# Kernel tuning notes

Measured on AMD Instinct MI355X. Metric: run time of the kernel, lower is better.

## Reference

```python
import jax, jax.numpy as jnp
import numpy as np

# ---- fixed config (Linear_mvm defaults, XBAR 64x64) ----
ROW = 64; COL = 64
BIT_SLICE = 2; BIT_STREAM = 1
W_BITS = 16; W_FRAC = 12          # weight_bit_frac = weight_bits//4*3
I_BITS = 16; I_FRAC = 12          # input_bit_frac  = input_bits//4*3
ADC_BIT = 8                       # log2(ROW) + bit_slice (bit_stream==1)
ACM_BITS = 16; ACM_FRAC = 12
BSN = W_BITS // BIT_SLICE         # 8 slices per weight, MSB-first columns
STN = I_BITS // BIT_STREAM        # 16 input bit-streams, LSB-first
IN_F = 1024; OUT_F = 1024; BATCH = 256


def _bit_slice_weight(w_nonneg):
    # w_nonneg: [out, in] nonnegative -> sliced crossbar matrix [in, out*BSN] (MSB->LSB per channel)
    w_int = jnp.clip(jnp.round(w_nonneg * (2.0 ** W_FRAC)), 0.0, 2.0 ** W_BITS - 1.0)
    shifts = (BIT_SLICE * (BSN - 1 - jnp.arange(BSN))).astype(jnp.float32)
    sl = jnp.floor(w_int[..., None] / (2.0 ** shifts)) % (2 ** BIT_SLICE)  # [out,in,BSN]
    o, i = w_nonneg.shape
    return sl.transpose(1, 0, 2).reshape(i, o * BSN)


def _input_bits(x):
    # two's-complement fixed point, LSB-first bit planes: [b, in, STN]
    x_int = jnp.clip(jnp.round(x * (2.0 ** I_FRAC)), -(2.0 ** (I_BITS - 1)), 2.0 ** (I_BITS - 1) - 1.0)
    x_u = jnp.where(x_int < 0, x_int + 2.0 ** I_BITS, x_int)
    return jnp.floor(x_u[..., None] / (2.0 ** jnp.arange(I_BITS, dtype=jnp.float32))) % 2.0


def _tile(mat, r, c):
    # pad to tile multiples and reshape to [xr, xc, r, c]
    pr = (-mat.shape[0]) % r; pc = (-mat.shape[1]) % c
    m = jnp.pad(mat, ((0, pr), (0, pc)))
    xr, xc = m.shape[0] // r, m.shape[1] // c
    return m.reshape(xr, r, xc, c).transpose(0, 2, 1, 3)


def _adc(a):
    # uniform ADC quantization of the analog column current to ADC_BIT bits
    full = float(ROW * (2 ** BIT_SLICE - 1))
    step = full / (2.0 ** ADC_BIT - 1.0)
    return jnp.clip(jnp.round(a / step) * step, 0.0, full)


def _mvm_one_sign(bits_tiled, xbars):
    # bits_tiled [b, xr, ROW, STN]; xbars [xr, xc, ROW, COL]
    sw_slice = 2.0 ** (BIT_SLICE * (BSN - 1 - jnp.arange(BSN, dtype=jnp.float32)))  # MSB..LSB
    sw_stream = 2.0 ** (BIT_STREAM * jnp.arange(STN, dtype=jnp.float32))
    sw_stream = sw_stream.at[-1].multiply(-1.0)  # two's-complement MSB stream

    def step(acc, si):
        bi, w = si                                   # bi [b,xr,ROW]
        analog = jnp.einsum('brk,rckj->brcj', bi, xbars)  # [b,xr,xc,COL]
        analog = _adc(analog)
        b, xr, xc, _ = analog.shape
        dig = analog.reshape(b, xr, xc, COL // BSN, BSN) @ sw_slice  # shift-add slices
        return acc + w * dig, None

    b = bits_tiled.shape[0]; xr, xc = xbars.shape[0], xbars.shape[1]
    acc0 = jnp.zeros((b, xr, xc, COL // BSN), jnp.float32)
    streams = jnp.moveaxis(bits_tiled, -1, 0)  # [STN, b, xr, ROW]
    acc, _ = jax.lax.scan(step, acc0, (streams, sw_stream))
    return acc.sum(axis=1).reshape(b, xc * (COL // BSN))  # sum row tiles, flatten channels


def _forward(x, weight, bias):
    pos = _bit_slice_weight(jnp.maximum(weight, 0.0))
    neg = _bit_slice_weight(-jnp.minimum(weight, 0.0))
    xb_pos = _tile(pos, ROW, COL)
    xb_neg = _tile(neg, ROW, COL)
    bits = _input_bits(x)                                  # [b,in,STN]
    xr = xb_pos.shape[0]
    bits = jnp.pad(bits, ((0, 0), (0, xr * ROW - bits.shape[1]), (0, 0)))
    bits = bits.reshape(x.shape[0], xr, ROW, STN)
    out = _mvm_one_sign(bits, xb_pos) - _mvm_one_sign(bits, xb_neg)
    out = out * (2.0 ** (-(W_FRAC + I_FRAC)))              # undo fixed-point scaling
    # accumulator quantization to ACM_BITS / ACM_FRAC
    out = jnp.clip(jnp.round(out * 2.0 ** ACM_FRAC), -(2.0 ** (ACM_BITS - 1)), 2.0 ** (ACM_BITS - 1) - 1.0) * 2.0 ** (-ACM_FRAC)
    out = out[:, :OUT_F]
    return out + bias[None, :]


def setup_inputs() -> dict:
    key = jax.random.key(0)
    k1, k2, k3 = jax.random.split(key, 3)
    x = jax.random.normal(k1, (BATCH, IN_F), jnp.float32)
    weight = jax.random.normal(k2, (OUT_F, IN_F), jnp.float32) * 0.05  # representable in Q4.12
    bias = jax.random.normal(k3, (OUT_F,), jnp.float32) * 0.05
    return {"x": x, "weight": weight, "bias": bias}


def reference(x, weight, bias):
    return _forward(x, weight, bias)
```

## Files before the change

### kernel.cpp

```cpp
#include <hip/hip_runtime.h>
#include <stdint.h>

#define BATCH 256
#define IN_F  1024
#define OUT_F 1024
#define RT    16
#define STN   16
#define NCOL  16384

typedef int   v4i  __attribute__((ext_vector_type(4)));
typedef int   v16i __attribute__((ext_vector_type(16)));
typedef float v2f  __attribute__((ext_vector_type(2)));

#define AP_SZ ((size_t)STN * BATCH * IN_F)
#define BP_SZ ((size_t)64 * NCOL * 16)

__global__ __launch_bounds__(256) void pack_fused(
    const float* __restrict__ x, const float* __restrict__ w,
    uint8_t* __restrict__ Ap2, uint8_t* __restrict__ Bp,
    uint32_t* __restrict__ flags)
{
    if (blockIdx.x < 512) {
        int item = blockIdx.x * 256 + threadIdx.x;
        int o  = item & 1023;
        int sg = (item >> 10) & 1;
        int g  = item >> 11;
        const float* wr = w + (size_t)o * IN_F + g * 16;
        uint32_t wq[16];
        #pragma unroll
        for (int j = 0; j < 16; ++j) {
            float wv = wr[j];
            float wf = rintf(fmaxf(sg ? -wv : wv, 0.0f) * 4096.0f);
            wq[j] = (uint32_t)fminf(wf, 65535.0f);
        }
        uint32_t nzmask = 0;
        #pragma unroll
        for (int s = 0; s < 8; ++s) {
            int sh = 14 - 2 * s;
            uint32_t dw[4], nz = 0;
            #pragma unroll
            for (int q = 0; q < 4; ++q) {
                uint32_t d = 0;
                #pragma unroll
                for (int j = 0; j < 4; ++j)
                    d |= ((wq[q * 4 + j] >> sh) & 3u) << (8 * j);
                dw[q] = d;
                nz |= d;
            }
            int sgs = sg * 8 + s;
            *(uint4*)(Bp + (size_t)(g * NCOL + sgs * 1024 + o) * 16) =
                make_uint4(dw[0], dw[1], dw[2], dw[3]);
            nzmask |= (nz ? 1u : 0u) << s;
        }
        int r = g >> 2, ob = o >> 7;
        #pragma unroll
        for (int s = 0; s < 8; ++s) {
            int any = __any((int)((nzmask >> s) & 1u));
            if (any && (threadIdx.x & 63) == 0)
                atomicOr(&flags[(sg * 8 + s) * 8 + ob], 1u << r);
        }
    } else {
        int item = (blockIdx.x - 512) * 256 + threadIdx.x;
        int b  = item & 255;
        int tq = (item >> 8) & 3;
        int kg = item >> 10;
        int r = kg >> 2, f = (kg >> 1) & 1, hi = kg & 1;
        int y = b >> 5, l = hi * 32 + (b & 31);
        const float* xr = x + (size_t)b * IN_F + kg * 16;
        uint32_t xu[16];
        #pragma unroll
        for (int j = 0; j < 16; ++j) {
            float xf = rintf(xr[j] * 4096.0f);
            xf = fminf(fmaxf(xf, -32768.0f), 32767.0f);
            xu[j] = (uint32_t)((int)xf) & 0xFFFFu;
        }
        uint8_t* wbase = Ap2 + ((size_t)(r * 8 + y) * 16) * 2048 + f * 1024 + l * 16;
        #pragma unroll
        for (int tt = 0; tt < 4; ++tt) {
            int t = tq * 4 + tt;
            uint32_t dw[4];
            #pragma unroll
            for (int q = 0; q < 4; ++q) {
                uint32_t d = 0;
                #pragma unroll
                for (int j = 0; j < 4; ++j)
                    d |= ((xu[q * 4 + j] >> t) & 1u) << (8 * j);
                dw[q] = d;
            }
            *(uint4*)(wbase + t * 2048) = make_uint4(dw[0], dw[1], dw[2], dw[3]);
        }
    }
}

__global__ __launch_bounds__(512) void cim_block(
    const uint8_t* __restrict__ Ap2, const uint8_t* __restrict__ Bp,
    const uint32_t* __restrict__ flags, const float* __restrict__ bias,
    float* __restrict__ out)
{
    __shared__ float red[8 * 1024];
    const float MAG = 12582912.0f;
    int tid = threadIdx.x, wid = tid >> 6, l = tid & 63, h2 = l >> 5;
    int oq = blockIdx.x, y = blockIdx.y;
    int ob = oq >> 2;

    uint32_t fw = flags[(l & 15) * 8 + ob];

    v2f acc2[8];
    #pragma unroll
    for (int i = 0; i < 8; ++i) acc2[i] = (v2f)0.0f;
    v16i zero;
    #pragma unroll
    for (int i = 0; i < 16; ++i) zero[i] = 0;

    int cnt = 0;
    for (int r = 0; r < RT; ++r) {
        uint32_t smask = (uint32_t)(__ballot((int)((fw >> r) & 1u))) & 0xFFFFu;
        while (smask) {
            int sgs = __builtin_ctz(smask);
            smask &= smask - 1;
            if ((cnt++ & 7) != wid) continue;

            int s = sgs & 7, sg = sgs >> 3;
            float clane = __int_as_float((141 - 2 * s) << 23) * (192.0f / 255.0f);
            if (sg) clane = -clane;
            int col = sgs * 1024 + oq * 32 + (l & 31);

            v4i bf0 = *(const v4i*)(Bp + ((size_t)(r * 4 + h2)     * NCOL + col) * 16);
            v4i bf1 = *(const v4i*)(Bp + ((size_t)(r * 4 + 2 + h2) * NCOL + col) * 16);

            const uint8_t* abase = Ap2 + ((size_t)(r * 8 + y) * 16) * 2048 + l * 16;
            #pragma unroll 4
            for (int t = 0; t < STN; ++t) {
                const uint8_t* ap = abase + t * 2048;
                v4i af0 = *(const v4i*)ap;
                v4i af1 = *(const v4i*)(ap + 1024);
                v16i c = __builtin_amdgcn_mfma_i32_32x32x32_i8(af0, bf0, zero, 0, 0, 0);
                c      = __builtin_amdgcn_mfma_i32_32x32x32_i8(af1, bf1, c,    0, 0, 0);
                float wt = (t == 15) ? -32768.0f : (float)(1 << t);
                float cw = clane * wt;
                #pragma unroll
                for (int i = 0; i < 8; ++i) {
                    v2f af; af.x = (float)c[2 * i]; af.y = (float)c[2 * i + 1];
                    v2f tq;
                    tq.x = fmaf(af.x, 1.328125f, MAG);
                    tq.y = fmaf(af.y, 1.328125f, MAG);
                    v2f qf = tq - MAG;
                    acc2[i].x = fmaf(qf.x, cw, acc2[i].x);
                    acc2[i].y = fmaf(qf.y, cw, acc2[i].y);
                }
            }
        }
    }

    float* slot = red + wid * 1024 + l * 16;
    #pragma unroll
    for (int i = 0; i < 8; ++i) {
        slot[2 * i]     = acc2[i].x;
        slot[2 * i + 1] = acc2[i].y;
    }
    __syncthreads();
    #pragma unroll
    for (int k = 0; k < 2; ++k) {
        int e = k * 512 + tid;
        float v = 0.0f;
        #pragma unroll
        for (int w = 0; w < 8; ++w) v += red[w * 1024 + e];
        int ll = e >> 4, i = e & 15;
        int b = y * 32 + (i & 3) + 8 * (i >> 2) + 4 * (ll >> 5);
        int o = oq * 32 + (ll & 31);
        float ov = v * 0x1p-24f;
        float q = rintf(ov * 4096.0f);
        q = fminf(fmaxf(q, -32768.0f), 32767.0f);
        out[(size_t)b * OUT_F + o] = q * 0x1p-12f + bias[o];
    }
}

extern "C" void kernel_launch(void* const* d_in, const int* in_sizes, int n_in,
                              void* d_out, int out_size, void* d_ws, size_t ws_size,
                              hipStream_t stream) {
    const float* x    = (const float*)d_in[0];
    const float* w    = (const float*)d_in[1];
    const float* bias = (const float*)d_in[2];
    float* out = (float*)d_out;

    uint8_t*  Ap2   = (uint8_t*)d_ws;
    uint8_t*  Bp    = Ap2 + AP_SZ;
    uint32_t* flags = (uint32_t*)(Bp + BP_SZ);

    hipMemsetAsync(flags, 0, 128 * sizeof(uint32_t), stream);
    hipLaunchKernelGGL(pack_fused, dim3(768), dim3(256), 0, stream,
                       x, w, Ap2, Bp, flags);
    hipLaunchKernelGGL(cim_block, dim3(32, 8), dim3(512), 0, stream,
                       Ap2, Bp, flags, bias, out);
}
```

Measured before the change: 175.3 us.

## Double-buffer input bit planes in LDS and refine sparsity flags to 32-column granularity

The MFMA kernel now stages each row tile's input bit-plane block into double-buffered LDS with global_load_lds, prefetching the next active row tile while computing the current one, instead of reloading A fragments from global memory in every wave. Skip flags move from 128-column to 32-column granularity, so each block tests only its own columns and skips whole row tiles with no nonzero slices. The reduction buffer reuses the LDS staging space with a transposed layout. This adds a block-wide barrier per row tile, which could serialise waves whose work is unbalanced.

```diff
diff --git a/kernel.cpp b/kernel.cpp
--- a/kernel.cpp
+++ b/kernel.cpp
@@ -25,6 +25,7 @@
         int o  = item & 1023;
         int sg = (item >> 10) & 1;
         int g  = item >> 11;
+        int l  = threadIdx.x & 63;
         const float* wr = w + (size_t)o * IN_F + g * 16;
         uint32_t wq[16];
         #pragma unroll
@@ -52,12 +53,14 @@
                 make_uint4(dw[0], dw[1], dw[2], dw[3]);
             nzmask |= (nz ? 1u : 0u) << s;
         }
-        int r = g >> 2, ob = o >> 7;
+        int r = g >> 2;
         #pragma unroll
         for (int s = 0; s < 8; ++s) {
-            int any = __any((int)((nzmask >> s) & 1u));
-            if (any && (threadIdx.x & 63) == 0)
-                atomicOr(&flags[(sg * 8 + s) * 8 + ob], 1u << r);
+            unsigned long long bal = __ballot((int)((nzmask >> s) & 1u));
+            uint32_t lo = (uint32_t)bal, hi = (uint32_t)(bal >> 32);
+            int sgs = sg * 8 + s;
+            if (l == 0 && lo)  atomicOr(&flags[sgs * 32 + (o >> 5)], 1u << r);
+            if (l == 32 && hi) atomicOr(&flags[sgs * 32 + (o >> 5)], 1u << r);
         }
     } else {
         int item = (blockIdx.x - 512) * 256 + threadIdx.x;
@@ -97,13 +100,16 @@
     const uint32_t* __restrict__ flags, const float* __restrict__ bias,
     float* __restrict__ out)
 {
-    __shared__ float red[8 * 1024];
+    __shared__ __align__(16) uint8_t Abuf[2][32768];
     const float MAG = 12582912.0f;
     int tid = threadIdx.x, wid = tid >> 6, l = tid & 63, h2 = l >> 5;
     int oq = blockIdx.x, y = blockIdx.y;
-    int ob = oq >> 2;
-
-    uint32_t fw = flags[(l & 15) * 8 + ob];
+
+    uint32_t fw = flags[(l & 15) * 32 + oq];
+    uint32_t rmask = fw;
+    #pragma unroll
+    for (int st = 1; st < 16; st <<= 1)
+        rmask |= __shfl_xor(rmask, st, 64);
 
     v2f acc2[8];
     #pragma unroll
@@ -112,9 +118,32 @@
     #pragma unroll
     for (int i = 0; i < 16; ++i) zero[i] = 0;
 
-    int cnt = 0;
-    for (int r = 0; r < RT; ++r) {
-        uint32_t smask = (uint32_t)(__ballot((int)((fw >> r) & 1u))) & 0xFFFFu;
+    #define STAGE(BUF, R)                                                     \
+        do {                                                                  \
+            const uint8_t* sbase = Ap2 + (size_t)((R) * 8 + y) * 32768;       \
+            _Pragma("unroll")                                                 \
+            for (int ii = 0; ii < 4; ++ii) {                                  \
+                int chunk = wid * 4 + ii;                                     \
+                __builtin_amdgcn_global_load_lds(                             \
+                    (const __attribute__((address_space(1))) uint32_t*)       \
+                        (sbase + chunk * 1024 + l * 16),                      \
+                    (__attribute__((address_space(3))) uint32_t*)             \
+                        (&Abuf[BUF][0] + chunk * 1024),                       \
+                    16, 0, 0);                                                \
+            }                                                                 \
+        } while (0)
+
+    int cnt = 0, cur = 0;
+    uint32_t rm = rmask;
+    if (rm) STAGE(0, __builtin_ctz(rm));
+    __syncthreads();
+
+    while (rm) {
+        int r = __builtin_ctz(rm);
+        rm &= rm - 1;
+        if (rm) STAGE(cur ^ 1, __builtin_ctz(rm));
+
+        uint32_t smask = (uint32_t)__ballot((int)((fw >> r) & 1u)) & 0xFFFFu;
         while (smask) {
             int sgs = __builtin_ctz(smask);
             smask &= smask - 1;
@@ -128,12 +157,11 @@
             v4i bf0 = *(const v4i*)(Bp + ((size_t)(r * 4 + h2)     * NCOL + col) * 16);
             v4i bf1 = *(const v4i*)(Bp + ((size_t)(r * 4 + 2 + h2) * NCOL + col) * 16);
 
-            const uint8_t* abase = Ap2 + ((size_t)(r * 8 + y) * 16) * 2048 + l * 16;
+            const uint8_t* abase = &Abuf[cur][0] + l * 16;
             #pragma unroll 4
             for (int t = 0; t < STN; ++t) {
-                const uint8_t* ap = abase + t * 2048;
-                v4i af0 = *(const v4i*)ap;
-                v4i af1 = *(const v4i*)(ap + 1024);
+                v4i af0 = *(const v4i*)(abase + t * 2048);
+                v4i af1 = *(const v4i*)(abase + t * 2048 + 1024);
                 v16i c = __builtin_amdgcn_mfma_i32_32x32x32_i8(af0, bf0, zero, 0, 0, 0);
                 c      = __builtin_amdgcn_mfma_i32_32x32x32_i8(af1, bf1, c,    0, 0, 0);
                 float wt = (t == 15) ? -32768.0f : (float)(1 << t);
@@ -149,25 +177,28 @@
                     acc2[i].y = fmaf(qf.y, cw, acc2[i].y);
                 }
             }
-        }
-    }
-
-    float* slot = red + wid * 1024 + l * 16;
-    #pragma unroll
-    for (int i = 0; i < 8; ++i) {
-        slot[2 * i]     = acc2[i].x;
-        slot[2 * i + 1] = acc2[i].y;
-    }
+            __asm__ volatile("" ::: "memory");
+        }
+        __syncthreads();
+        cur ^= 1;
+    }
+
+    float* red = (float*)&Abuf[0][0];
     __syncthreads();
     #pragma unroll
+    for (int i = 0; i < 16; ++i) {
+        float v = (i & 1) ? acc2[i >> 1].y : acc2[i >> 1].x;
+        red[wid * 1024 + i * 64 + l] = v;
+    }
+    __syncthreads();
+    #pragma unroll
     for (int k = 0; k < 2; ++k) {
-        int e = k * 512 + tid;
+        int i = wid * 2 + k;
         float v = 0.0f;
         #pragma unroll
-        for (int w = 0; w < 8; ++w) v += red[w * 1024 + e];
-        int ll = e >> 4, i = e & 15;
-        int b = y * 32 + (i & 3) + 8 * (i >> 2) + 4 * (ll >> 5);
-        int o = oq * 32 + (ll & 31);
+        for (int w8 = 0; w8 < 8; ++w8) v += red[w8 * 1024 + i * 64 + l];
+        int b = y * 32 + (i & 3) + 8 * (i >> 2) + 4 * h2;
+        int o = oq * 32 + (l & 31);
         float ov = v * 0x1p-24f;
         float q = rintf(ov * 4096.0f);
         q = fminf(fmaxf(q, -32768.0f), 32767.0f);
@@ -187,7 +218,7 @@
     uint8_t*  Bp    = Ap2 + AP_SZ;
     uint32_t* flags = (uint32_t*)(Bp + BP_SZ);
 
-    hipMemsetAsync(flags, 0, 128 * sizeof(uint32_t), stream);
+    hipMemsetAsync(flags, 0, 512 * sizeof(uint32_t), stream);
     hipLaunchKernelGGL(pack_fused, dim3(768), dim3(256), 0, stream,
                        x, w, Ap2, Bp, flags);
     hipLaunchKernelGGL(cim_block, dim3(32, 8), dim3(512), 0, stream,
```

Result: slower. 191.6 us (+9.3%).
